# Performance work log

Measured on AMD Instinct MI355X. Metric: run time of the kernel, lower is better.

The kernel has to match this reference:

```python
import jax, jax.numpy as jnp
import numpy as np

D_IN = 1024
D_OUT = 1024
SEQ = 4096


def setup_inputs() -> dict:
    key = jax.random.key(0)
    kx, kq, kk, kv = jax.random.split(key, 4)
    x = jax.random.normal(kx, (SEQ, D_IN), dtype=jnp.float32)
    # torch.rand -> uniform [0,1)
    wquery = jax.random.uniform(kq, (D_IN, D_OUT), dtype=jnp.float32)
    wkey = jax.random.uniform(kk, (D_IN, D_OUT), dtype=jnp.float32)
    wvalue = jax.random.uniform(kv, (D_IN, D_OUT), dtype=jnp.float32)
    return {"x": x, "wquery": wquery, "wkey": wkey, "wvalue": wvalue}


def reference(x, wquery, wkey, wvalue):
    keys = x @ wkey          # [S, d_out]
    queries = x @ wquery     # [S, d_out]
    values = x @ wvalue      # [S, d_out]
    scale = 1.0 / jnp.sqrt(jnp.float32(keys.shape[-1]))
    attn_scores = queries @ keys.T            # [S, S]
    attn_weights = jax.nn.softmax(attn_scores * scale, axis=-1)
    context = attn_weights @ values           # [S, d_out]
    return context
```

## Files before the change

kernel.cpp:

```cpp
#include <hip/hip_runtime.h>
#include <math.h>

#define SEQ 4096
#define DIM 1024

typedef _Float16 f16;
typedef _Float16 f16x8 __attribute__((ext_vector_type(8)));
typedef _Float16 f16x4 __attribute__((ext_vector_type(4)));
typedef float f32x4 __attribute__((ext_vector_type(4)));

#define GLOAD_LDS16(g, l)                                              \
    __builtin_amdgcn_global_load_lds(                                  \
        (const __attribute__((address_space(1))) void*)(g),            \
        (__attribute__((address_space(3))) void*)(l), 16, 0, 0)

__global__ __launch_bounds__(256) void split16rs(const float* __restrict__ in,
                                                 f16* __restrict__ hi,
                                                 f16* __restrict__ lo,
                                                 float* __restrict__ sx) {
    __shared__ float sred[4];
    const int tid = threadIdx.x;
    const int i = blockIdx.x * 256 + tid;
    const float4 v = ((const float4*)in)[i];
    const float vv[4] = {v.x, v.y, v.z, v.w};
    f16x4 h, l;
#pragma unroll
    for (int q = 0; q < 4; ++q) {
        const f16 hq = (f16)vv[q];
        h[q] = hq;
        l[q] = (f16)(vv[q] - (float)hq);
    }
    ((f16x4*)hi)[i] = h;
    ((f16x4*)lo)[i] = l;
    float s = v.x + v.y + v.z + v.w;
#pragma unroll
    for (int m = 32; m >= 1; m >>= 1) s += __shfl_xor(s, m);
    if ((tid & 63) == 0) sred[tid >> 6] = s;
    __syncthreads();
    if (tid == 0) sx[blockIdx.x] = sred[0] + sred[1] + sred[2] + sred[3];
}

__global__ __launch_bounds__(256) void wtrans3h(
    const float* __restrict__ Wq, const float* __restrict__ Wk,
    const float* __restrict__ Wv,
    f16* __restrict__ QT, f16* __restrict__ KT, f16* __restrict__ VT) {
    __shared__ float tile[32][33];
    const int tid = threadIdx.x;
    const int r0 = blockIdx.x * 32;
    const int c0 = blockIdx.y * 32;
    const int z = blockIdx.z;
    const float* W = (z == 0) ? Wq : (z == 1) ? Wk : Wv;
    f16* T = (z == 0) ? QT : (z == 1) ? KT : VT;
    const float off = (z < 2) ? 0.5f : 0.0f;
    {
        const int r = tid >> 3, c = (tid & 7) * 4;
        const float4 v = *(const float4*)&W[(size_t)(r0 + r) * DIM + c0 + c];
        tile[r][c + 0] = v.x;
        tile[r][c + 1] = v.y;
        tile[r][c + 2] = v.z;
        tile[r][c + 3] = v.w;
    }
    __syncthreads();
    {
        const int n = tid >> 3;
        const int k = (tid & 7) * 4;
        f16x4 h;
#pragma unroll
        for (int q = 0; q < 4; ++q) h[q] = (f16)(tile[k + q][n] - off);
        *(f16x4*)&T[(size_t)(c0 + n) * DIM + r0 + k] = h;
    }
}

#define EPI_F32 0
#define EPI_SPLIT16 1
#define EPI_TRANS16 2

template <int NPAIR, int KTILES>
__global__ __launch_bounds__(256, 2) void gemm128s(
    const f16* __restrict__ A0, const f16* __restrict__ A1, int ldA, int ldB,
    const f16* __restrict__ B0_0, const f16* __restrict__ B1_0,
    void* o0_0, void* o1_0,
    const f16* __restrict__ B0_1, const f16* __restrict__ B1_1,
    void* o0_1, void* o1_1,
    const f16* __restrict__ B0_2, const f16* __restrict__ B1_2,
    void* o0_2, void* o1_2,
    float* rs0, float* rs1,
    int epi0, int epi1, int epi2,
    int N, float scale) {
    __shared__ __align__(16) f16 As[2][128 * 64];
    __shared__ __align__(16) f16 Bs[2][128 * 64];

    const int tid = threadIdx.x;
    const int lane = tid & 63;
    const int wid = tid >> 6;
    const int wr = wid >> 1, wc = wid & 1;

    const int total = (int)(gridDim.y << 5);
    int lid = (int)blockIdx.y * 32 + (int)blockIdx.x;
    lid = (lid & 7) * (total >> 3) + (lid >> 3);
    const int bx = lid & 31;
    int by = lid >> 5;

    const int set = by >> 3;
    by &= 7;

    const f16 *B0, *B1;
    void *o0, *o1;
    int epi;
    float* rs;
    if (set == 0)      { B0 = B0_0; B1 = B1_0; o0 = o0_0; o1 = o1_0; epi = epi0; rs = rs0; }
    else if (set == 1) { B0 = B0_1; B1 = B1_1; o0 = o0_1; o1 = o1_1; epi = epi1; rs = rs1; }
    else               { B0 = B0_2; B1 = B1_2; o0 = o0_2; o1 = o1_2; epi = epi2; rs = nullptr; }

    const int m0 = bx * 128;
    const int n0 = by * 128;

    const f16* APs[2] = {A0, A1};
    const f16* BPs[2] = {B0, B1};
    const int nt = NPAIR * KTILES;

    f32x4 acc[4][4];
#pragma unroll
    for (int i = 0; i < 4; ++i)
#pragma unroll
        for (int j = 0; j < 4; ++j) acc[i][j] = (f32x4){0.f, 0.f, 0.f, 0.f};

    auto STAGE = [&](int t, int b) {
        const int pass = t / KTILES;
        const int k0 = (t % KTILES) * 64;
        const f16* Ap = APs[pass];
        const f16* Bp = BPs[pass];
#pragma unroll
        for (int L = 0; L < 4; ++L) {
            const int idx = L * 256 + tid;
            const int row = idx >> 3;
            const int sc = ((idx & 7) * 16) ^ ((row & 7) << 4);
            const int ldsu = (L * 256 + (tid & ~63)) * 8;
            GLOAD_LDS16(Ap + (size_t)(m0 + row) * ldA + k0 + (sc >> 1),
                        &As[b][ldsu]);
            GLOAD_LDS16(Bp + (size_t)(n0 + row) * ldB + k0 + (sc >> 1),
                        &Bs[b][ldsu]);
        }
    };

    STAGE(0, 0);

    for (int t = 0; t < nt; ++t) {
        const int cur = t & 1;
        __builtin_amdgcn_s_barrier();
        asm volatile("" ::: "memory");
        if (t + 1 < nt) {
            STAGE(t + 1, cur ^ 1);
            asm volatile("s_waitcnt vmcnt(8)" ::: "memory");
        } else {
            asm volatile("s_waitcnt vmcnt(0)" ::: "memory");
        }
        __builtin_amdgcn_s_barrier();
        asm volatile("" ::: "memory");

#pragma unroll
        for (int kk = 0; kk < 2; ++kk) {
            const int cb = kk * 64 + (lane >> 4) * 16;
            f16x8 af[4], bv[4];
#pragma unroll
            for (int i = 0; i < 4; ++i) {
                const int r = wr * 64 + i * 16 + (lane & 15);
                af[i] = *(const f16x8*)(&As[cur][r * 64 +
                                                 ((cb ^ ((r & 7) << 4)) >> 1)]);
            }
#pragma unroll
            for (int j = 0; j < 4; ++j) {
                const int r = wc * 64 + j * 16 + (lane & 15);
                bv[j] = *(const f16x8*)(&Bs[cur][r * 64 +
                                                 ((cb ^ ((r & 7) << 4)) >> 1)]);
            }
            __builtin_amdgcn_s_setprio(1);
#pragma unroll
            for (int i = 0; i < 4; ++i)
#pragma unroll
                for (int j = 0; j < 4; ++j)
                    acc[i][j] = __builtin_amdgcn_mfma_f32_16x16x32_f16(
                        af[i], bv[j], acc[i][j], 0, 0, 0);
            __builtin_amdgcn_s_setprio(0);
        }
    }

    const int row0 = m0 + wr * 64 + (lane >> 4) * 4;
    const int col0 = n0 + wc * 64 + (lane & 15);

    if (epi == EPI_F32) {
        float* O = (float*)o0;
#pragma unroll
        for (int i = 0; i < 4; ++i)
#pragma unroll
            for (int j = 0; j < 4; ++j)
#pragma unroll
                for (int q = 0; q < 4; ++q)
                    O[(size_t)(row0 + i * 16 + q) * N + col0 + j * 16] =
                        acc[i][j][q] * scale;
    } else if (epi == EPI_SPLIT16) {
        f16* Hi = (f16*)o0;
        f16* Lo = (f16*)o1;
#pragma unroll
        for (int i = 0; i < 4; ++i)
#pragma unroll
            for (int j = 0; j < 4; ++j)
#pragma unroll
                for (int q = 0; q < 4; ++q) {
                    const float x = acc[i][j][q];
                    const f16 h = (f16)x;
                    const size_t idx = (size_t)(row0 + i * 16 + q) * N + col0 + j * 16;
                    Hi[idx] = h;
                    if (Lo) Lo[idx] = (f16)(x - (float)h);
                }
        if (rs) {
#pragma unroll
            for (int i = 0; i < 4; ++i)
#pragma unroll
                for (int q = 0; q < 4; ++q) {
                    float rsum = acc[i][0][q] + acc[i][1][q] +
                                 acc[i][2][q] + acc[i][3][q];
#pragma unroll
                    for (int msk = 1; msk < 16; msk <<= 1)
                        rsum += __shfl_xor(rsum, msk);
                    if ((lane & 15) == 0)
                        atomicAdd(&rs[row0 + i * 16 + q], rsum);
                }
        }
    } else {
        f16* OT = (f16*)o0;
#pragma unroll
        for (int i = 0; i < 4; ++i)
#pragma unroll
            for (int j = 0; j < 4; ++j) {
                f16x4 v;
#pragma unroll
                for (int q = 0; q < 4; ++q) v[q] = (f16)acc[i][j][q];
                *(f16x4*)&OT[(size_t)(col0 + j * 16) * SEQ + row0 + i * 16] = v;
            }
    }
}

template <int NPAIR, int KT>
__global__ __launch_bounds__(512, 2) void qkrank1(
    const f16* __restrict__ A0, const f16* __restrict__ B0,
    const f16* __restrict__ A1, const f16* __restrict__ B1,
    const float* __restrict__ sx, const float* __restrict__ rq,
    const float* __restrict__ rk,
    f16* __restrict__ Pu, float* __restrict__ Mp, float* __restrict__ Lp) {
    constexpr int K = KT * 64;
    constexpr int nt = NPAIR * KT;
    __shared__ __align__(16) f16 As[2][256 * 64];
    __shared__ __align__(16) f16 Bs[2][256 * 64];

    const int tid = threadIdx.x;
    const int lane = tid & 63;
    const int wid = tid >> 6;
    const int wr = wid >> 2;
    const int wc = wid & 3;

    const int wg = ((int)blockIdx.x & 7) * 32 + ((int)blockIdx.x >> 3);
    const int m0 = (wg >> 4) * 256;
    const int n0 = (wg & 15) * 256;
    const int bcol = n0 >> 8;

    const f16* APs[2] = {A0, A1};
    const f16* BPs[2] = {B0, B1};

    f32x4 acc[8][4];
#pragma unroll
    for (int i = 0; i < 8; ++i)
#pragma unroll
        for (int j = 0; j < 4; ++j) acc[i][j] = (f32x4){0.f, 0.f, 0.f, 0.f};

    auto STAGE = [&](int t, int b) {
        const f16* Ap = APs[t / KT];
        const f16* Bp = BPs[t / KT];
        const int k0 = (t % KT) * 64;
#pragma unroll
        for (int L = 0; L < 4; ++L) {
            const int idx = L * 512 + tid;
            const int row = idx >> 3;
            const int sc = ((idx & 7) * 16) ^ ((row & 7) << 4);
            const int ldsu = (L * 512 + (tid & ~63)) * 8;
            GLOAD_LDS16(Ap + (size_t)(m0 + row) * K + k0 + (sc >> 1),
                        &As[b][ldsu]);
            GLOAD_LDS16(Bp + (size_t)(n0 + row) * K + k0 + (sc >> 1),
                        &Bs[b][ldsu]);
        }
    };

    STAGE(0, 0);

    for (int t = 0; t < nt; ++t) {
        const int cur = t & 1;
        __builtin_amdgcn_s_barrier();
        asm volatile("" ::: "memory");
        if (t + 1 < nt) {
            STAGE(t + 1, cur ^ 1);
            asm volatile("s_waitcnt vmcnt(8)" ::: "memory");
        } else {
            asm volatile("s_waitcnt vmcnt(0)" ::: "memory");
        }
        __builtin_amdgcn_s_barrier();
        asm volatile("" ::: "memory");

#pragma unroll
        for (int kk = 0; kk < 2; ++kk) {
            const int cb = kk * 64 + (lane >> 4) * 16;
            f16x8 af[8], bv[4];
#pragma unroll
            for (int i = 0; i < 8; ++i) {
                const int r = wr * 128 + i * 16 + (lane & 15);
                af[i] = *(const f16x8*)(&As[cur][r * 64 +
                                                 ((cb ^ ((r & 7) << 4)) >> 1)]);
            }
#pragma unroll
            for (int j = 0; j < 4; ++j) {
                const int r = wc * 64 + j * 16 + (lane & 15);
                bv[j] = *(const f16x8*)(&Bs[cur][r * 64 +
                                                 ((cb ^ ((r & 7) << 4)) >> 1)]);
            }
            __builtin_amdgcn_s_setprio(1);
#pragma unroll
            for (int i = 0; i < 8; ++i)
#pragma unroll
                for (int j = 0; j < 4; ++j)
                    acc[i][j] = __builtin_amdgcn_mfma_f32_16x16x32_f16(
                        af[i], bv[j], acc[i][j], 0, 0, 0);
            __builtin_amdgcn_s_setprio(0);
        }
    }

    const int g4 = lane >> 4;
    const int l15 = lane & 15;
    const int row0 = m0 + wr * 128 + g4 * 4;
    const int col0 = n0 + wc * 64 + l15;
    float u[4], w4[4];
#pragma unroll
    for (int j = 0; j < 4; ++j) {
        const float sxc = sx[col0 + j * 16];
        u[j] = 256.f * sxc + 0.5f * rk[col0 + j * 16];
        w4[j] = 0.5f * sxc;
    }
#pragma unroll
    for (int i = 0; i < 8; ++i)
#pragma unroll
        for (int q = 0; q < 4; ++q) {
            const int r = row0 + i * 16 + q;
            const float sxr = sx[r];
            const float rqr = rq[r];
#pragma unroll
            for (int j = 0; j < 4; ++j)
                acc[i][j][q] =
                    (acc[i][j][q] + sxr * u[j] + rqr * w4[j]) * 0.03125f;
        }

    float* partm = (float*)&As[0][0];
    float* mrow  = partm + 1024;
    float* parts = mrow + 256;
    float red[8][4];
#pragma unroll
    for (int i = 0; i < 8; ++i)
#pragma unroll
        for (int q = 0; q < 4; ++q) {
            float v = acc[i][0][q];
#pragma unroll
            for (int j = 1; j < 4; ++j) v = fmaxf(v, acc[i][j][q]);
            red[i][q] = v;
        }
#pragma unroll
    for (int msk = 1; msk < 16; msk <<= 1)
#pragma unroll
        for (int i = 0; i < 8; ++i)
#pragma unroll
            for (int q = 0; q < 4; ++q)
                red[i][q] = fmaxf(red[i][q], __shfl_xor(red[i][q], msk));
    __syncthreads();
    if (l15 == 0)
#pragma unroll
        for (int i = 0; i < 8; ++i)
#pragma unroll
            for (int q = 0; q < 4; ++q)
                partm[(wr * 128 + i * 16 + g4 * 4 + q) * 4 + wc] = red[i][q];
    __syncthreads();
    if (tid < 256) {
        const float* p = partm + tid * 4;
        mrow[tid] = fmaxf(fmaxf(p[0], p[1]), fmaxf(p[2], p[3]));
    }
    __syncthreads();
#pragma unroll
    for (int i = 0; i < 8; ++i)
#pragma unroll
        for (int q = 0; q < 4; ++q) {
            const float mB = mrow[wr * 128 + i * 16 + g4 * 4 + q];
            float s = 0.f;
#pragma unroll
            for (int j = 0; j < 4; ++j) {
                const float e = __expf(acc[i][j][q] - mB);
                acc[i][j][q] = e;
                s += e;
            }
            red[i][q] = s;
        }
#pragma unroll
    for (int msk = 1; msk < 16; msk <<= 1)
#pragma unroll
        for (int i = 0; i < 8; ++i)
#pragma unroll
            for (int q = 0; q < 4; ++q) red[i][q] += __shfl_xor(red[i][q], msk);
    if (l15 == 0)
#pragma unroll
        for (int i = 0; i < 8; ++i)
#pragma unroll
            for (int q = 0; q < 4; ++q)
                parts[(wr * 128 + i * 16 + g4 * 4 + q) * 4 + wc] = red[i][q];
    __syncthreads();
    if (tid < 256) {
        const float* p = parts + tid * 4;
        Mp[(size_t)(m0 + tid) * 16 + bcol] = mrow[tid];
        Lp[(size_t)(m0 + tid) * 16 + bcol] = p[0] + p[1] + p[2] + p[3];
    }
#pragma unroll
    for (int i = 0; i < 8; ++i)
#pragma unroll
        for (int q = 0; q < 4; ++q) {
            const size_t r = row0 + i * 16 + q;
#pragma unroll
            for (int j = 0; j < 4; ++j)
                Pu[r * SEQ + col0 + j * 16] = (f16)acc[i][j][q];
        }
}

__global__ __launch_bounds__(256) void mkD(const float* __restrict__ Mp,
                                           const float* __restrict__ Lp,
                                           float* __restrict__ D) {
    const size_t r = blockIdx.x * 256 + threadIdx.x;
    float mv[16], lv[16];
#pragma unroll
    for (int b = 0; b < 16; ++b) mv[b] = Mp[r * 16 + b];
#pragma unroll
    for (int b = 0; b < 16; ++b) lv[b] = Lp[r * 16 + b];
    float m = mv[0];
#pragma unroll
    for (int b = 1; b < 16; ++b) m = fmaxf(m, mv[b]);
    float l = 0.f;
#pragma unroll
    for (int b = 0; b < 16; ++b) l += __expf(mv[b] - m) * lv[b];
    const float inv = 1.f / l;
#pragma unroll
    for (int b = 0; b < 16; ++b) D[r * 16 + b] = __expf(mv[b] - m) * inv;
}

template <int KTILES>
__global__ __launch_bounds__(256, 2) void pvstrip(
    const f16* __restrict__ Pu, const f16* __restrict__ VT,
    const float* __restrict__ D,
    float* __restrict__ P0, float* __restrict__ P1) {
    __shared__ __align__(16) f16 As[2][128 * 64];
    __shared__ __align__(16) f16 Bs[2][128 * 64];

    const int tid = threadIdx.x;
    const int lane = tid & 63;
    const int wid = tid >> 6;
    const int wr = wid >> 1, wc = wid & 1;

    const int total = (int)(gridDim.y << 5);
    int lid = (int)blockIdx.y * 32 + (int)blockIdx.x;
    lid = (lid & 7) * (total >> 3) + (lid >> 3);
    const int bx = lid & 31;
    int by = lid >> 5;
    const int set = by >> 3;
    by &= 7;
    float* Out = set ? P1 : P0;
    const int koff = set * 2048;
    const int strip0 = set * 8;

    const int m0 = bx * 128;
    const int n0 = by * 128;
    const int row0 = m0 + wr * 64 + (lane >> 4) * 4;
    const int col0 = n0 + wc * 64 + (lane & 15);

    f32x4 acc[4][4], acc2[4][4];
#pragma unroll
    for (int i = 0; i < 4; ++i)
#pragma unroll
        for (int j = 0; j < 4; ++j) {
            acc[i][j] = (f32x4){0.f, 0.f, 0.f, 0.f};
            acc2[i][j] = (f32x4){0.f, 0.f, 0.f, 0.f};
        }

    auto STAGE = [&](int t, int b) {
        const int k0 = t * 64 + koff;
#pragma unroll
        for (int L = 0; L < 4; ++L) {
            const int idx = L * 256 + tid;
            const int row = idx >> 3;
            const int sc = ((idx & 7) * 16) ^ ((row & 7) << 4);
            const int ldsu = (L * 256 + (tid & ~63)) * 8;
            GLOAD_LDS16(Pu + (size_t)(m0 + row) * SEQ + k0 + (sc >> 1),
                        &As[b][ldsu]);
            GLOAD_LDS16(VT + (size_t)(n0 + row) * SEQ + k0 + (sc >> 1),
                        &Bs[b][ldsu]);
        }
    };

    STAGE(0, 0);

    for (int t = 0; t < KTILES; ++t) {
        const int cur = t & 1;
        __builtin_amdgcn_s_barrier();
        asm volatile("" ::: "memory");
        if (t + 1 < KTILES) {
            STAGE(t + 1, cur ^ 1);
            asm volatile("s_waitcnt vmcnt(8)" ::: "memory");
        } else {
            asm volatile("s_waitcnt vmcnt(0)" ::: "memory");
        }
        __builtin_amdgcn_s_barrier();
        asm volatile("" ::: "memory");

#pragma unroll
        for (int kk = 0; kk < 2; ++kk) {
            const int cb = kk * 64 + (lane >> 4) * 16;
            f16x8 af[4], bv[4];
#pragma unroll
            for (int i = 0; i < 4; ++i) {
                const int r = wr * 64 + i * 16 + (lane & 15);
                af[i] = *(const f16x8*)(&As[cur][r * 64 +
                                                 ((cb ^ ((r & 7) << 4)) >> 1)]);
            }
#pragma unroll
            for (int j = 0; j < 4; ++j) {
                const int r = wc * 64 + j * 16 + (lane & 15);
                bv[j] = *(const f16x8*)(&Bs[cur][r * 64 +
                                                 ((cb ^ ((r & 7) << 4)) >> 1)]);
            }
            __builtin_amdgcn_s_setprio(1);
#pragma unroll
            for (int i = 0; i < 4; ++i)
#pragma unroll
                for (int j = 0; j < 4; ++j)
                    acc[i][j] = __builtin_amdgcn_mfma_f32_16x16x32_f16(
                        af[i], bv[j], acc[i][j], 0, 0, 0);
            __builtin_amdgcn_s_setprio(0);
        }

        if ((t & 3) == 3) {
            const int strip = strip0 + (t >> 2);
#pragma unroll
            for (int i = 0; i < 4; ++i)
#pragma unroll
                for (int q = 0; q < 4; ++q) {
                    const float dv = D[(size_t)(row0 + i * 16 + q) * 16 + strip];
#pragma unroll
                    for (int j = 0; j < 4; ++j) {
                        acc2[i][j][q] += dv * acc[i][j][q];
                        acc[i][j][q] = 0.f;
                    }
                }
        }
    }

#pragma unroll
    for (int i = 0; i < 4; ++i)
#pragma unroll
        for (int j = 0; j < 4; ++j)
#pragma unroll
            for (int q = 0; q < 4; ++q)
                Out[(size_t)(row0 + i * 16 + q) * DIM + col0 + j * 16] =
                    acc2[i][j][q];
}

__global__ __launch_bounds__(256) void addf(const float* __restrict__ a,
                                            const float* __restrict__ b,
                                            float* __restrict__ o) {
    const int i = blockIdx.x * 256 + threadIdx.x;
    const float4 x = ((const float4*)a)[i];
    const float4 y = ((const float4*)b)[i];
    ((float4*)o)[i] = make_float4(x.x + y.x, x.y + y.y, x.z + y.z, x.w + y.w);
}

extern "C" void kernel_launch(void* const* d_in, const int* in_sizes, int n_in,
                              void* d_out, int out_size, void* d_ws, size_t ws_size,
                              hipStream_t stream) {
    const float* x  = (const float*)d_in[0];
    const float* wq = (const float*)d_in[1];
    const float* wk = (const float*)d_in[2];
    const float* wv = (const float*)d_in[3];
    float* O = (float*)d_out;

    char* ws = (char*)d_ws;
    const size_t MB = 1024 * 1024;
    const size_t KB = 1024;
    f16* Qh = (f16*)(ws + 0 * MB);
    f16* Ql = (f16*)(ws + 8 * MB);
    f16* Kh = (f16*)(ws + 16 * MB);
    f16* VT = (f16*)(ws + 24 * MB);
    float* sx = (float*)(ws + 32 * MB);
    float* rq = (float*)(ws + 32 * MB + 16 * KB);
    float* rk = (float*)(ws + 32 * MB + 32 * KB);
    float* Mp = (float*)(ws + 32 * MB + 48 * KB);
    float* Lp = (float*)(ws + 32 * MB + 304 * KB);
    float* D  = (float*)(ws + 33 * MB);
    f16* Pu = (f16*)(ws + 40 * MB);
    float* P0 = (float*)(ws + 72 * MB);
    float* P1 = (float*)(ws + 88 * MB);
    f16* Xh  = (f16*)(ws + 40 * MB);
    f16* Xl  = (f16*)(ws + 48 * MB);
    f16* Wqh = (f16*)(ws + 56 * MB);
    f16* Wkh = (f16*)(ws + 58 * MB);
    f16* Wvh = (f16*)(ws + 60 * MB);

    split16rs<<<4096, 256, 0, stream>>>(x, Xh, Xl, sx);
    wtrans3h<<<dim3(DIM / 32, DIM / 32, 3), 256, 0, stream>>>(
        wq, wk, wv, Wqh, Wkh, Wvh);

    hipMemsetAsync(rq, 0, 32 * KB, stream);

    gemm128s<2, 16><<<dim3(32, 24), 256, 0, stream>>>(
        Xh, Xl, DIM, DIM,
        Wqh, Wqh, Qh, Ql,
        Wkh, Wkh, Kh, nullptr,
        Wvh, Wvh, VT, nullptr,
        rq, rk,
        EPI_SPLIT16, EPI_SPLIT16, EPI_TRANS16,
        DIM, 1.f);

    qkrank1<2, 16><<<256, 512, 0, stream>>>(
        Qh, Kh, Ql, Kh, sx, rq, rk, Pu, Mp, Lp);

    mkD<<<16, 256, 0, stream>>>(Mp, Lp, D);

    pvstrip<32><<<dim3(32, 16), 256, 0, stream>>>(Pu, VT, D, P0, P1);

    addf<<<4096, 256, 0, stream>>>(P0, P1, O);
}
```

Before: 224.9 us.

## Fuse prep kernels, fold softmax normalizer into PV, atomically reduce split-K output

Merges the x split and the weight transpose kernels into one launch, indexed by a flat block id. Each PV block now computes its own softmax normalization factors into LDS from Mp/Lp, which removes the separate mkD kernel. The final add of the two split-K partial outputs is replaced by float atomicAdd into a zeroed output, removing the addf kernel and the P0/P1 buffers. This cuts launch overhead and 32MB of partial-output traffic, at the cost of a 16MB memset, atomic contention between two writers per element, and summation order that is no longer deterministic.

```diff
diff --git a/kernel.cpp b/kernel.cpp
--- a/kernel.cpp
+++ b/kernel.cpp
@@ -14,41 +14,44 @@
         (const __attribute__((address_space(1))) void*)(g),            \
         (__attribute__((address_space(3))) void*)(l), 16, 0, 0)
 
-__global__ __launch_bounds__(256) void split16rs(const float* __restrict__ in,
-                                                 f16* __restrict__ hi,
-                                                 f16* __restrict__ lo,
-                                                 float* __restrict__ sx) {
+__global__ __launch_bounds__(256) void prep(
+    const float* __restrict__ x,
+    const float* __restrict__ Wq, const float* __restrict__ Wk,
+    const float* __restrict__ Wv,
+    f16* __restrict__ Xh, f16* __restrict__ Xl, float* __restrict__ sx,
+    f16* __restrict__ QT, f16* __restrict__ KT, f16* __restrict__ VT) {
+    __shared__ float tile[32][33];
     __shared__ float sred[4];
     const int tid = threadIdx.x;
-    const int i = blockIdx.x * 256 + tid;
-    const float4 v = ((const float4*)in)[i];
-    const float vv[4] = {v.x, v.y, v.z, v.w};
-    f16x4 h, l;
-#pragma unroll
-    for (int q = 0; q < 4; ++q) {
-        const f16 hq = (f16)vv[q];
-        h[q] = hq;
-        l[q] = (f16)(vv[q] - (float)hq);
-    }
-    ((f16x4*)hi)[i] = h;
-    ((f16x4*)lo)[i] = l;
-    float s = v.x + v.y + v.z + v.w;
-#pragma unroll
-    for (int m = 32; m >= 1; m >>= 1) s += __shfl_xor(s, m);
-    if ((tid & 63) == 0) sred[tid >> 6] = s;
-    __syncthreads();
-    if (tid == 0) sx[blockIdx.x] = sred[0] + sred[1] + sred[2] + sred[3];
-}
-
-__global__ __launch_bounds__(256) void wtrans3h(
-    const float* __restrict__ Wq, const float* __restrict__ Wk,
-    const float* __restrict__ Wv,
-    f16* __restrict__ QT, f16* __restrict__ KT, f16* __restrict__ VT) {
-    __shared__ float tile[32][33];
-    const int tid = threadIdx.x;
-    const int r0 = blockIdx.x * 32;
-    const int c0 = blockIdx.y * 32;
-    const int z = blockIdx.z;
+    const int bid = blockIdx.x;
+
+    if (bid < 4096) {
+        const int i = bid * 256 + tid;
+        const float4 v = ((const float4*)x)[i];
+        const float vv[4] = {v.x, v.y, v.z, v.w};
+        f16x4 h, l;
+#pragma unroll
+        for (int q = 0; q < 4; ++q) {
+            const f16 hq = (f16)vv[q];
+            h[q] = hq;
+            l[q] = (f16)(vv[q] - (float)hq);
+        }
+        ((f16x4*)Xh)[i] = h;
+        ((f16x4*)Xl)[i] = l;
+        float s = v.x + v.y + v.z + v.w;
+#pragma unroll
+        for (int m = 32; m >= 1; m >>= 1) s += __shfl_xor(s, m);
+        if ((tid & 63) == 0) sred[tid >> 6] = s;
+        __syncthreads();
+        if (tid == 0) sx[bid] = sred[0] + sred[1] + sred[2] + sred[3];
+        return;
+    }
+
+    const int w = bid - 4096;
+    const int z = w >> 10;
+    const int idx = w & 1023;
+    const int r0 = (idx >> 5) * 32;
+    const int c0 = (idx & 31) * 32;
     const float* W = (z == 0) ? Wq : (z == 1) ? Wk : Wv;
     f16* T = (z == 0) ? QT : (z == 1) ? KT : VT;
     const float off = (z < 2) ? 0.5f : 0.0f;
@@ -432,33 +435,14 @@
         }
 }
 
-__global__ __launch_bounds__(256) void mkD(const float* __restrict__ Mp,
-                                           const float* __restrict__ Lp,
-                                           float* __restrict__ D) {
-    const size_t r = blockIdx.x * 256 + threadIdx.x;
-    float mv[16], lv[16];
-#pragma unroll
-    for (int b = 0; b < 16; ++b) mv[b] = Mp[r * 16 + b];
-#pragma unroll
-    for (int b = 0; b < 16; ++b) lv[b] = Lp[r * 16 + b];
-    float m = mv[0];
-#pragma unroll
-    for (int b = 1; b < 16; ++b) m = fmaxf(m, mv[b]);
-    float l = 0.f;
-#pragma unroll
-    for (int b = 0; b < 16; ++b) l += __expf(mv[b] - m) * lv[b];
-    const float inv = 1.f / l;
-#pragma unroll
-    for (int b = 0; b < 16; ++b) D[r * 16 + b] = __expf(mv[b] - m) * inv;
-}
-
 template <int KTILES>
 __global__ __launch_bounds__(256, 2) void pvstrip(
     const f16* __restrict__ Pu, const f16* __restrict__ VT,
-    const float* __restrict__ D,
-    float* __restrict__ P0, float* __restrict__ P1) {
+    const float* __restrict__ Mp, const float* __restrict__ Lp,
+    float* __restrict__ O) {
     __shared__ __align__(16) f16 As[2][128 * 64];
     __shared__ __align__(16) f16 Bs[2][128 * 64];
+    __shared__ float Dl[128][8];
 
     const int tid = threadIdx.x;
     const int lane = tid & 63;
@@ -472,7 +456,6 @@
     int by = lid >> 5;
     const int set = by >> 3;
     by &= 7;
-    float* Out = set ? P1 : P0;
     const int koff = set * 2048;
     const int strip0 = set * 8;
 
@@ -507,6 +490,25 @@
 
     STAGE(0, 0);
 
+    if (tid < 128) {
+        const size_t r = m0 + tid;
+        float mv[16];
+        float m = -1e30f;
+#pragma unroll
+        for (int b = 0; b < 16; ++b) {
+            mv[b] = Mp[r * 16 + b];
+            m = fmaxf(m, mv[b]);
+        }
+        float l = 0.f;
+#pragma unroll
+        for (int b = 0; b < 16; ++b) l += __expf(mv[b] - m) * Lp[r * 16 + b];
+        const float inv = 1.f / l;
+#pragma unroll
+        for (int s = 0; s < 8; ++s)
+            Dl[tid][s] = __expf(mv[strip0 + s] - m) * inv;
+    }
+    __syncthreads();
+
     for (int t = 0; t < KTILES; ++t) {
         const int cur = t & 1;
         __builtin_amdgcn_s_barrier();
@@ -547,12 +549,13 @@
         }
 
         if ((t & 3) == 3) {
-            const int strip = strip0 + (t >> 2);
+            const int s = t >> 2;
+            const int lr0 = wr * 64 + ((lane >> 4)) * 4;
 #pragma unroll
             for (int i = 0; i < 4; ++i)
 #pragma unroll
                 for (int q = 0; q < 4; ++q) {
-                    const float dv = D[(size_t)(row0 + i * 16 + q) * 16 + strip];
+                    const float dv = Dl[lr0 + i * 16 + q][s];
 #pragma unroll
                     for (int j = 0; j < 4; ++j) {
                         acc2[i][j][q] += dv * acc[i][j][q];
@@ -568,17 +571,8 @@
         for (int j = 0; j < 4; ++j)
 #pragma unroll
             for (int q = 0; q < 4; ++q)
-                Out[(size_t)(row0 + i * 16 + q) * DIM + col0 + j * 16] =
-                    acc2[i][j][q];
-}
-
-__global__ __launch_bounds__(256) void addf(const float* __restrict__ a,
-                                            const float* __restrict__ b,
-                                            float* __restrict__ o) {
-    const int i = blockIdx.x * 256 + threadIdx.x;
-    const float4 x = ((const float4*)a)[i];
-    const float4 y = ((const float4*)b)[i];
-    ((float4*)o)[i] = make_float4(x.x + y.x, x.y + y.y, x.z + y.z, x.w + y.w);
+                atomicAdd(&O[(size_t)(row0 + i * 16 + q) * DIM + col0 + j * 16],
+                          acc2[i][j][q]);
 }
 
 extern "C" void kernel_launch(void* const* d_in, const int* in_sizes, int n_in,
@@ -602,21 +596,18 @@
     float* rk = (float*)(ws + 32 * MB + 32 * KB);
     float* Mp = (float*)(ws + 32 * MB + 48 * KB);
     float* Lp = (float*)(ws + 32 * MB + 304 * KB);
-    float* D  = (float*)(ws + 33 * MB);
     f16* Pu = (f16*)(ws + 40 * MB);
-    float* P0 = (float*)(ws + 72 * MB);
-    float* P1 = (float*)(ws + 88 * MB);
     f16* Xh  = (f16*)(ws + 40 * MB);
     f16* Xl  = (f16*)(ws + 48 * MB);
     f16* Wqh = (f16*)(ws + 56 * MB);
     f16* Wkh = (f16*)(ws + 58 * MB);
     f16* Wvh = (f16*)(ws + 60 * MB);
 
-    split16rs<<<4096, 256, 0, stream>>>(x, Xh, Xl, sx);
-    wtrans3h<<<dim3(DIM / 32, DIM / 32, 3), 256, 0, stream>>>(
-        wq, wk, wv, Wqh, Wkh, Wvh);
-
+    hipMemsetAsync(O, 0, (size_t)SEQ * DIM * 4, stream);
     hipMemsetAsync(rq, 0, 32 * KB, stream);
+
+    prep<<<4096 + 3072, 256, 0, stream>>>(x, wq, wk, wv, Xh, Xl, sx,
+                                          Wqh, Wkh, Wvh);
 
     gemm128s<2, 16><<<dim3(32, 24), 256, 0, stream>>>(
         Xh, Xl, DIM, DIM,
@@ -630,9 +621,5 @@
     qkrank1<2, 16><<<256, 512, 0, stream>>>(
         Qh, Kh, Ql, Kh, sx, rq, rk, Pu, Mp, Lp);
 
-    mkD<<<16, 256, 0, stream>>>(Mp, Lp, D);
-
-    pvstrip<32><<<dim3(32, 16), 256, 0, stream>>>(Pu, VT, D, P0, P1);
-
-    addf<<<4096, 256, 0, stream>>>(P0, P1, O);
+    pvstrip<32><<<dim3(32, 16), 256, 0, stream>>>(Pu, VT, Mp, Lp, O);
 }
```

Result: slower. 237.4 us (+5.5%).
